# Optimization experiments

Measured on AMD Instinct MI355X. Metric: run time of the kernel, lower is better.

Reference implementation:

```python
import jax, jax.numpy as jnp
import numpy as np

B_COMMITMENT = 1.0


def setup_inputs() -> dict:
    key = jax.random.key(0)
    k1, k2 = jax.random.split(key)
    inpt = jax.random.normal(k1, (16, 1024, 256), dtype=jnp.float32)
    emb_mtrx = jax.random.normal(k2, (256, 8192), dtype=jnp.float32) * 0.05
    return {"inpt": inpt, "emb_mtrx": emb_mtrx}


def reference(inpt, emb_mtrx):
    D = inpt.shape[-1]
    x = inpt.reshape(-1, D)  # [N, D]
    # squared L2 distance to every code: [N, K]
    dist = (
        jnp.sum(x * x, axis=1, keepdims=True)
        - 2.0 * (x @ emb_mtrx)
        + jnp.sum(emb_mtrx * emb_mtrx, axis=0, keepdims=True)
    )
    idx = jnp.argmin(dist, axis=1).reshape(inpt.shape[:-1])  # [B, T]
    q = jnp.take(emb_mtrx.T, idx, axis=0)  # [B, T, D] gather of nearest codes
    l_commitment = jnp.mean((jax.lax.stop_gradient(q) - inpt) ** 2)
    l_codebook = jnp.mean((q - jax.lax.stop_gradient(inpt)) ** 2)
    loss = B_COMMITMENT * l_commitment + l_codebook
    q_st = inpt + jax.lax.stop_gradient(q - inpt)  # straight-through
    return q_st, loss
```

## Files before the change

kernel.cpp:

```cpp
#include <hip/hip_runtime.h>
#include <hip/hip_bf16.h>
#include <cstdint>


typedef __bf16 bf16x8 __attribute__((ext_vector_type(8)));
typedef __bf16 bf16x4 __attribute__((ext_vector_type(4)));
typedef float  f32x16 __attribute__((ext_vector_type(16)));

#define N_ROWS  16384
#define N_CODES 8192
#define DDIM    256
#define NT      16
#define BUFB3   32768
#define NMAX    8192
#define THETA   0.020f

#define P1_LDS   163840
#define P1_EOFF  131072
#define P1_NOFF  155648

#define STAGE16(gptr, lptr) __builtin_amdgcn_global_load_lds( \
    (const __attribute__((address_space(1))) void*)(gptr),    \
    (__attribute__((address_space(3))) void*)(lptr), 16, 0, 0)

#define SBAR() do { asm volatile("" ::: "memory"); \
                    __builtin_amdgcn_s_barrier();  \
                    asm volatile("" ::: "memory"); } while (0)
#define WAITVM(N) asm volatile("s_waitcnt vmcnt(" #N ")" ::: "memory")
#define LGKM0() do { asm volatile("s_waitcnt lgkmcnt(0)" ::: "memory"); \
                     __builtin_amdgcn_sched_barrier(0); } while (0)

__device__ __forceinline__ unsigned mapf(float f) {
  unsigned u = __float_as_uint(f);
  return (u & 0x80000000u) ? ~u : (u | 0x80000000u);
}
__device__ __forceinline__ float unmapf(unsigned u) {
  u = (u & 0x80000000u) ? (u & 0x7fffffffu) : ~u;
  return __uint_as_float(u);
}

__global__ void prep_all_k(const float* __restrict__ x, const float* __restrict__ emb,
                           __bf16* __restrict__ xhi, __bf16* __restrict__ xlo,
                           __bf16* __restrict__ ehi, __bf16* __restrict__ elo,
                           float* __restrict__ enorm) {
  __shared__ float tile[64][65];
  const int b = blockIdx.x;
  const int t = threadIdx.x;
  if (b < 4096) {
    int i = b * 256 + t;
    float4 v = reinterpret_cast<const float4*>(x)[i];
    float a[4] = {v.x, v.y, v.z, v.w};
    bf16x4 h, l;
#pragma unroll
    for (int j = 0; j < 4; ++j) {
      __bf16 hh = (__bf16)a[j];
      h[j] = hh;
      l[j] = (__bf16)(a[j] - (float)hh);
    }
    reinterpret_cast<bf16x4*>(xhi)[i] = h;
    reinterpret_cast<bf16x4*>(xlo)[i] = l;
  } else if (b < 4608) {
    const int pb = b - 4096;
    const int kb = (pb & 127) * 64, db = (pb >> 7) * 64;
    const int tk = t & 63, td = t >> 6;
#pragma unroll
    for (int c = 0; c < 16; ++c) {
      int d = c * 4 + td;
      tile[d][tk] = emb[(size_t)(db + d) * N_CODES + kb + tk];
    }
    __syncthreads();
#pragma unroll
    for (int c = 0; c < 16; ++c) {
      int k = c * 4 + td;
      int d = tk;
      float v = tile[d][k];
      size_t o = (size_t)(kb + k) * DDIM + db + d;
      __bf16 h = (__bf16)v;
      ehi[o] = h;
      elo[o] = (__bf16)(v - (float)h);
    }
  } else {
    int k = (b - 4608) * 256 + t;
    float s = 0.f;
    for (int d = 0; d < DDIM; ++d) {
      float v = emb[(size_t)d * N_CODES + k];
      s += v * v;
    }
    enorm[k] = s;
  }
}

__global__ __launch_bounds__(512, 2) void pass1_k(
    const __bf16* __restrict__ xhi, const __bf16* __restrict__ ehi,
    const float* __restrict__ enorm,
    unsigned long long* __restrict__ k2k, float* __restrict__ k2v) {
  extern __shared__ __align__(16) unsigned char smem[];

  const int tid = threadIdx.x;
  const int wid = tid >> 6, lane = tid & 63;
  const int cg = wid >> 2, rg = wid & 3;
  const int l31 = lane & 31, lh = lane >> 5;

  const int bm = blockIdx.x >> 2;
  const int bnq = blockIdx.x & 3;

  unsigned char* xr = smem;
  unsigned char* eb = smem + P1_EOFF;
  float* enf = (float*)(smem + P1_NOFF);

  const size_t xsrc = (size_t)(bm * 256 + wid * 32 + l31) * 512 + (size_t)lh * 16;
#pragma unroll
  for (int kc = 0; kc < 16; ++kc)
    STAGE16((const char*)xhi + xsrc + kc * 32, xr + (kc * 8 + wid) * 1024);
  STAGE16((const char*)enorm + bnq * 8192 + wid * 1024 + lane * 16,
          smem + P1_NOFF + wid * 1024);
  const size_t esrc0 = (size_t)(bnq * 8 * 256 + wid * 32 + l31) * 512 + (size_t)lh * 16;
  STAGE16((const char*)ehi + esrc0, eb + wid * 1024);
  STAGE16((const char*)ehi + esrc0 + 32, eb + 8192 + wid * 1024);
  WAITVM(1);
  SBAR();

  const int erd = cg * 4096 + lane * 16;

  f32x16 acc[4][2];
#define INIT_ACC(BI) do {                                                      \
  _Pragma("unroll")                                                            \
  for (int c_ = 0; c_ < 4; ++c_) {                                             \
    f32x16 ci_;                                                                \
    _Pragma("unroll")                                                          \
    for (int q_ = 0; q_ < 4; ++q_) {                                           \
      float4 v4_ = *(const float4*)(enf + (BI) * 256 + cg * 128 + c_ * 32 +    \
                                    q_ * 8 + lh * 4);                          \
      ci_[q_ * 4 + 0] = -0.5f * v4_.x; ci_[q_ * 4 + 1] = -0.5f * v4_.y;        \
      ci_[q_ * 4 + 2] = -0.5f * v4_.z; ci_[q_ * 4 + 3] = -0.5f * v4_.w;        \
    }                                                                          \
    acc[c_][0] = ci_; acc[c_][1] = ci_;                                        \
  } } while (0)
  INIT_ACC(0);

  const int rowl = rg * 64 + l31;

#pragma unroll 1
  for (int g = 0; g < 128; ++g) {
    const int s = (g + 2) & 127;
    const size_t esrc = (size_t)((bnq * 8 + (s >> 4)) * 256 + wid * 32 + l31) * 512 +
                        (size_t)(s & 15) * 32 + (size_t)lh * 16;
    STAGE16((const char*)ehi + esrc, eb + ((g + 2) % 3) * 8192 + wid * 1024);

    const unsigned char* rbuf = eb + (g % 3) * 8192;
    const unsigned char* xk = xr + (g & 15) * 8192;
    bf16x8 ef[4], xf[2];
#pragma unroll
    for (int c = 0; c < 4; ++c) ef[c] = *(const bf16x8*)(rbuf + erd + c * 1024);
#pragma unroll
    for (int r = 0; r < 2; ++r)
      xf[r] = *(const bf16x8*)(xk + (rg * 2 + r) * 1024 + lane * 16);

    __builtin_amdgcn_s_setprio(1);
#pragma unroll
    for (int c = 0; c < 4; ++c)
#pragma unroll
      for (int r = 0; r < 2; ++r)
        acc[c][r] = __builtin_amdgcn_mfma_f32_32x32x16_bf16(ef[c], xf[r], acc[c][r], 0, 0, 0);
    __builtin_amdgcn_s_setprio(0);

    WAITVM(1);
    SBAR();

    if ((g & 15) == 15) {
      const int bi = g >> 4;
      const int bn = bnq * 8 + bi;
      const int cbase = bn * 256 + cg * 128 + lh * 4;
      unsigned long long* ek = (unsigned long long*)(eb + (g % 3) * 8192);
      float* ev = (float*)(eb + (g % 3) * 8192 + 2048);
#pragma unroll
      for (int r = 0; r < 2; ++r) {
        float v1 = -3.4e38f, v2 = -3.4e38f;
        unsigned c1 = 0;
#pragma unroll
        for (int c = 0; c < 4; ++c)
#pragma unroll
          for (int q = 0; q < 4; ++q)
#pragma unroll
            for (int rr = 0; rr < 4; ++rr) {
              float v = acc[c][r][q * 4 + rr];
              unsigned cd = (unsigned)(cbase + c * 32 + q * 8 + rr);
              if (v > v1) { v2 = v1; v1 = v; c1 = cd; }
              else if (v > v2) v2 = v;
            }
        unsigned long long key =
            ((unsigned long long)mapf(v1) << 32) | (0xFFFFFFFFu ^ c1);
        unsigned klo = (unsigned)key, khi = (unsigned)(key >> 32);
        unsigned plo = __shfl_xor(klo, 32, 64), phi = __shfl_xor(khi, 32, 64);
        float pv1 = __shfl_xor(v1, 32, 64), pv2 = __shfl_xor(v2, 32, 64);
        unsigned long long pkey = ((unsigned long long)phi << 32) | plo;
        if (pkey > key) { v2 = fmaxf(v1, pv2); v1 = pv1; key = pkey; }
        else { v2 = fmaxf(pv1, v2); }
        SBAR();
        if (cg == 1 && lh == 0) { ek[rowl + r * 32] = key; ev[rowl + r * 32] = v2; }
        SBAR();
        if (cg == 0 && lh == 0) {
          unsigned long long pk = ek[rowl + r * 32];
          float ps2 = ev[rowl + r * 32];
          float nv2;
          if (pk > key) { nv2 = fmaxf(v1, ps2); key = pk; }
          else nv2 = fmaxf(unmapf((unsigned)(pk >> 32)), v2);
          const int grow = bm * 256 + rowl + r * 32;
          k2k[(size_t)bn * N_ROWS + grow] = key;
          k2v[(size_t)bn * N_ROWS + grow] = nv2;
        }
      }
      if (bi < 7) INIT_ACC(bi + 1);
      SBAR();
    }
  }
  WAITVM(0);
}

__global__ void reduce_k(const unsigned long long* __restrict__ k2k,
                         const float* __restrict__ k2v,
                         unsigned long long* __restrict__ keys,
                         unsigned* __restrict__ counter,
                         int* __restrict__ idxlist) {
  const int row = blockIdx.x * 256 + threadIdx.x;
  unsigned long long k = k2k[row];
  float s2 = k2v[row];
#pragma unroll 1
  for (int p = 1; p < 32; ++p) {
    unsigned long long kk = k2k[(size_t)p * N_ROWS + row];
    float ss2 = k2v[(size_t)p * N_ROWS + row];
    if (kk > k) { s2 = fmaxf(unmapf((unsigned)(k >> 32)), ss2); k = kk; }
    else        { s2 = fmaxf(unmapf((unsigned)(kk >> 32)), s2); }
  }
  float v1 = unmapf((unsigned)(k >> 32));
  if (v1 - s2 >= THETA) {
    keys[row] = k;
  } else {
    keys[row] = 0;
    unsigned pos = atomicAdd(counter, 1u);
    if (pos < NMAX) idxlist[pos] = row;
    else keys[row] = k;
  }
}

__global__ void compact_k(const __bf16* __restrict__ xhi, const __bf16* __restrict__ xlo,
                          const int* __restrict__ idxlist, const unsigned* __restrict__ counter,
                          __bf16* __restrict__ xch, __bf16* __restrict__ xcl) {
  const unsigned b = blockIdx.x;
  if (b >= *counter) return;
  const int row = idxlist[b];
  const int lane = threadIdx.x;
  reinterpret_cast<uint2*>(xch)[(size_t)b * 64 + lane] =
      reinterpret_cast<const uint2*>(xhi)[(size_t)row * 64 + lane];
  reinterpret_cast<uint2*>(xcl)[(size_t)b * 64 + lane] =
      reinterpret_cast<const uint2*>(xlo)[(size_t)row * 64 + lane];
}

__global__ __launch_bounds__(512, 2) void rescue_k(
    const __bf16* __restrict__ xch, const __bf16* __restrict__ xcl,
    const __bf16* __restrict__ ehi, const __bf16* __restrict__ elo,
    const float* __restrict__ enorm, unsigned long long* __restrict__ keys,
    const int* __restrict__ idxlist, const unsigned* __restrict__ counter) {
  extern __shared__ __align__(16) unsigned char smem[];

  const int bm = blockIdx.x >> 5;
  const int bn = blockIdx.x & 31;
  const unsigned nf = *counter;
  const int tiles = (int)((nf + 255u) >> 8);
  if (bm >= tiles) return;

  const int tid = threadIdx.x;
  const int wid = tid >> 6, lane = tid & 63;
  const int cg = wid >> 2, rg = wid & 3;
  const int l31 = lane & 31, lh = lane >> 5;

  const int cbase = bn * 256 + cg * 128 + lh * 4;
  f32x16 acc[4][2];
#pragma unroll
  for (int c = 0; c < 4; ++c) {
    f32x16 ci;
#pragma unroll
    for (int q = 0; q < 4; ++q)
#pragma unroll
      for (int r = 0; r < 4; ++r)
        ci[q * 4 + r] = -0.5f * enorm[cbase + c * 32 + q * 8 + r];
    acc[c][0] = ci; acc[c][1] = ci;
  }
  __builtin_amdgcn_sched_barrier(0);

  const size_t aoff = (size_t)(bm * 256 + wid * 32 + l31) * 512 + (size_t)lh * 16;
  const size_t boff = (size_t)(bn * 256 + wid * 32 + l31) * 512 + (size_t)lh * 16;
  const char* pxh = (const char*)xch + aoff;
  const char* pxl = (const char*)xcl + aoff;
  const char* peh = (const char*)ehi + boff;
  const char* pel = (const char*)elo + boff;
  const int dxh = wid * 1024, dxl = 8192 + wid * 1024;
  const int deh = 16384 + wid * 1024, del = 24576 + wid * 1024;

  const int xrd = rg * 2048 + lane * 16;
  const int erd = 16384 + cg * 4096 + lane * 16;

  unsigned char* b0 = smem;
  unsigned char* b1 = smem + BUFB3;
  unsigned char* b2 = smem + 2 * BUFB3;

  STAGE16(pxh, b0 + dxh); STAGE16(peh, b0 + deh);
  STAGE16(pxl, b0 + dxl); STAGE16(pel, b0 + del);
  STAGE16(pxh + 32, b1 + dxh); STAGE16(peh + 32, b1 + deh);
  STAGE16(pxl + 32, b1 + dxl); STAGE16(pel + 32, b1 + del);
  WAITVM(4);
  SBAR();

#pragma unroll 1
  for (int t = 0; t < NT; ++t) {
    int s = t + 2; if (s >= NT) s -= NT;
    const size_t kb = (size_t)s * 32;

    bf16x8 ehf[4], xhf[2];
#pragma unroll
    for (int c = 0; c < 4; ++c) ehf[c] = *(const bf16x8*)(b0 + erd + c * 1024);
#pragma unroll
    for (int r = 0; r < 2; ++r) xhf[r] = *(const bf16x8*)(b0 + xrd + r * 1024);
    STAGE16(pxh + kb, b2 + dxh);
    STAGE16(peh + kb, b2 + deh);
    SBAR();
    LGKM0();
    __builtin_amdgcn_s_setprio(1);
#pragma unroll
    for (int c = 0; c < 4; ++c)
#pragma unroll
      for (int r = 0; r < 2; ++r)
        acc[c][r] = __builtin_amdgcn_mfma_f32_32x32x16_bf16(ehf[c], xhf[r], acc[c][r], 0, 0, 0);
    __builtin_amdgcn_s_setprio(0);
    SBAR();

    bf16x8 xlf[2];
#pragma unroll
    for (int r = 0; r < 2; ++r) xlf[r] = *(const bf16x8*)(b0 + 8192 + xrd + r * 1024);
    STAGE16(pxl + kb, b2 + dxl);
    SBAR();
    LGKM0();
    __builtin_amdgcn_s_setprio(1);
#pragma unroll
    for (int c = 0; c < 4; ++c)
#pragma unroll
      for (int r = 0; r < 2; ++r)
        acc[c][r] = __builtin_amdgcn_mfma_f32_32x32x16_bf16(ehf[c], xlf[r], acc[c][r], 0, 0, 0);
    __builtin_amdgcn_s_setprio(0);
    SBAR();

    bf16x8 elf[4];
#pragma unroll
    for (int c = 0; c < 4; ++c) elf[c] = *(const bf16x8*)(b0 + 8192 + erd + c * 1024);
    STAGE16(pel + kb, b2 + del);
    SBAR();
    LGKM0();
    __builtin_amdgcn_s_setprio(1);
#pragma unroll
    for (int c = 0; c < 4; ++c)
#pragma unroll
      for (int r = 0; r < 2; ++r)
        acc[c][r] = __builtin_amdgcn_mfma_f32_32x32x16_bf16(elf[c], xhf[r], acc[c][r], 0, 0, 0);
    __builtin_amdgcn_s_setprio(0);
    WAITVM(4);
    SBAR();

    unsigned char* bt = b0; b0 = b1; b1 = b2; b2 = bt;
  }
  WAITVM(0);

#pragma unroll
  for (int r = 0; r < 2; ++r) {
    float bv = -3.4e38f;
    unsigned bcode = 0;
#pragma unroll
    for (int c = 0; c < 4; ++c)
#pragma unroll
      for (int q = 0; q < 4; ++q)
#pragma unroll
        for (int rr = 0; rr < 4; ++rr) {
          float v = acc[c][r][q * 4 + rr];
          unsigned cd = (unsigned)(cbase + c * 32 + q * 8 + rr);
          if (v > bv) { bv = v; bcode = cd; }
        }
    unsigned long long key =
        ((unsigned long long)mapf(bv) << 32) | (0xFFFFFFFFu ^ bcode);
    unsigned olo = __shfl_xor((unsigned)key, 32, 64);
    unsigned ohi = __shfl_xor((unsigned)(key >> 32), 32, 64);
    unsigned long long okey = ((unsigned long long)ohi << 32) | olo;
    if (okey > key) key = okey;
    const int crow = bm * 256 + rg * 64 + r * 32 + l31;
    if (lane < 32 && crow < (int)nf)
      atomicMax(&keys[idxlist[crow]], key);
  }
}

__global__ void gather_k(const float* __restrict__ x,
                         const __bf16* __restrict__ ehi, const __bf16* __restrict__ elo,
                         const unsigned long long* __restrict__ keys,
                         float* __restrict__ qout, float* __restrict__ rowsum) {
  const int row = blockIdx.x * 4 + (threadIdx.x >> 6);
  const int lane = threadIdx.x & 63;
  const unsigned low = (unsigned)(keys[row] & 0xffffffffull);
  const int idx = (int)(~low);
  ushort4 h4 = reinterpret_cast<const ushort4*>(ehi + (size_t)idx * DDIM)[lane];
  ushort4 l4 = reinterpret_cast<const ushort4*>(elo + (size_t)idx * DDIM)[lane];
  float4 xv = reinterpret_cast<const float4*>(x + (size_t)row * DDIM)[lane];
  float4 q;
  q.x = __uint_as_float((unsigned)h4.x << 16) + __uint_as_float((unsigned)l4.x << 16);
  q.y = __uint_as_float((unsigned)h4.y << 16) + __uint_as_float((unsigned)l4.y << 16);
  q.z = __uint_as_float((unsigned)h4.z << 16) + __uint_as_float((unsigned)l4.z << 16);
  q.w = __uint_as_float((unsigned)h4.w << 16) + __uint_as_float((unsigned)l4.w << 16);
  reinterpret_cast<float4*>(qout + (size_t)row * DDIM)[lane] = q;
  float dx = q.x - xv.x, dy = q.y - xv.y, dz = q.z - xv.z, dw = q.w - xv.w;
  float s = dx * dx + dy * dy + dz * dz + dw * dw;
#pragma unroll
  for (int mk = 32; mk; mk >>= 1) s += __shfl_xor(s, mk, 64);
  if (lane == 0) rowsum[row] = s;
}

__global__ void loss_k(const float* __restrict__ rowsum, float* __restrict__ out) {
  __shared__ float sm[4];
  const int t = threadIdx.x;
  float s = 0.f;
  for (int j = t; j < N_ROWS; j += 256) s += rowsum[j];
#pragma unroll
  for (int mk = 32; mk; mk >>= 1) s += __shfl_xor(s, mk, 64);
  if ((t & 63) == 0) sm[t >> 6] = s;
  __syncthreads();
  if (t == 0) out[0] = 2.0f * (sm[0] + sm[1] + sm[2] + sm[3]) / (float)(N_ROWS * DDIM);
}

extern "C" void kernel_launch(void* const* d_in, const int* in_sizes, int n_in,
                              void* d_out, int out_size, void* d_ws, size_t ws_size,
                              hipStream_t stream) {
  const float* x   = (const float*)d_in[0];
  const float* emb = (const float*)d_in[1];
  float* qout = (float*)d_out;

  char* w = (char*)d_ws;
  unsigned long long* keys = (unsigned long long*)w;
  float* rowsum   = (float*)(w + 131072);
  unsigned* counter = (unsigned*)(w + 196608);
  int* idxlist    = (int*)(w + 197632);
  __bf16* xhi     = (__bf16*)(w + 262144);
  __bf16* xlo     = xhi + (size_t)N_ROWS * DDIM;
  __bf16* ehi     = xlo + (size_t)N_ROWS * DDIM;
  __bf16* elo     = ehi + (size_t)N_CODES * DDIM;
  float*  enorm   = (float*)(elo + (size_t)N_CODES * DDIM);
  char*   k2base  = (char*)(enorm + N_CODES);
  unsigned long long* k2k = (unsigned long long*)k2base;
  float*  k2v     = (float*)(k2base + 4194304);
  __bf16* xch     = (__bf16*)k2base;
  __bf16* xcl     = (__bf16*)(k2base + 4194304);

  hipFuncSetAttribute((const void*)pass1_k,
                      hipFuncAttributeMaxDynamicSharedMemorySize, P1_LDS);
  hipFuncSetAttribute((const void*)rescue_k,
                      hipFuncAttributeMaxDynamicSharedMemorySize, 3 * BUFB3);

  hipMemsetAsync(counter, 0, sizeof(unsigned), stream);
  prep_all_k<<<4640, 256, 0, stream>>>(x, emb, xhi, xlo, ehi, elo, enorm);
  pass1_k<<<256, 512, P1_LDS, stream>>>(xhi, ehi, enorm, k2k, k2v);
  reduce_k<<<N_ROWS / 256, 256, 0, stream>>>(k2k, k2v, keys, counter, idxlist);
  compact_k<<<NMAX, 64, 0, stream>>>(xhi, xlo, idxlist, counter, xch, xcl);
  rescue_k<<<(NMAX / 256) * 32, 512, 3 * BUFB3, stream>>>(
      xch, xcl, ehi, elo, enorm, keys, idxlist, counter);
  gather_k<<<N_ROWS / 4, 256, 0, stream>>>(x, ehi, elo, keys, qout, rowsum);
  loss_k<<<1, 256, 0, stream>>>(rowsum, qout + (size_t)N_ROWS * DDIM);
}
```

Measured before the change: 203.9 us.

## Shrink pass1 tiles to 128 rows with 4 waves and double-buffered code staging

Pass1 now launches 512 blocks of 256 threads, each handling 128 input rows instead of 256, which halves the LDS footprint. Code-chunk staging drops from a triple buffer to a double buffer and waits for all loads before each barrier. The enorm values are read straight from global memory instead of being staged in LDS, and block indices are swizzled so neighbouring blocks share input rows. The aim is more resident blocks and better cache locality, at the cost of less reuse of each code tile per block and less prefetch slack.

```diff
diff --git a/kernel.cpp b/kernel.cpp
--- a/kernel.cpp
+++ b/kernel.cpp
@@ -15,9 +15,8 @@
 #define NMAX    8192
 #define THETA   0.020f
 
-#define P1_LDS   163840
-#define P1_EOFF  131072
-#define P1_NOFF  155648
+#define P1_LDS   81920
+#define P1_EOFF  65536
 
 #define STAGE16(gptr, lptr) __builtin_amdgcn_global_load_lds( \
     (const __attribute__((address_space(1))) void*)(gptr),    \
@@ -90,7 +89,7 @@
   }
 }
 
-__global__ __launch_bounds__(512, 2) void pass1_k(
+__global__ __launch_bounds__(256, 2) void pass1_k(
     const __bf16* __restrict__ xhi, const __bf16* __restrict__ ehi,
     const float* __restrict__ enorm,
     unsigned long long* __restrict__ k2k, float* __restrict__ k2v) {
@@ -98,39 +97,39 @@
 
   const int tid = threadIdx.x;
   const int wid = tid >> 6, lane = tid & 63;
-  const int cg = wid >> 2, rg = wid & 3;
+  const int rg = wid & 1, cg = wid >> 1;
   const int l31 = lane & 31, lh = lane >> 5;
 
-  const int bm = blockIdx.x >> 2;
-  const int bnq = blockIdx.x & 3;
+  const int orig = blockIdx.x;
+  const int j = orig >> 3;
+  const int bm = (orig & 7) * 16 + (j & 15);
+  const int bnq = j >> 4;
 
   unsigned char* xr = smem;
   unsigned char* eb = smem + P1_EOFF;
-  float* enf = (float*)(smem + P1_NOFF);
-
-  const size_t xsrc = (size_t)(bm * 256 + wid * 32 + l31) * 512 + (size_t)lh * 16;
+
+  const size_t xsrc = (size_t)(bm * 128 + wid * 32 + l31) * 512 + (size_t)lh * 16;
 #pragma unroll
   for (int kc = 0; kc < 16; ++kc)
-    STAGE16((const char*)xhi + xsrc + kc * 32, xr + (kc * 8 + wid) * 1024);
-  STAGE16((const char*)enorm + bnq * 8192 + wid * 1024 + lane * 16,
-          smem + P1_NOFF + wid * 1024);
-  const size_t esrc0 = (size_t)(bnq * 8 * 256 + wid * 32 + l31) * 512 + (size_t)lh * 16;
-  STAGE16((const char*)ehi + esrc0, eb + wid * 1024);
-  STAGE16((const char*)ehi + esrc0 + 32, eb + 8192 + wid * 1024);
-  WAITVM(1);
+    STAGE16((const char*)xhi + xsrc + kc * 32, xr + (kc * 4 + wid) * 1024);
+#pragma unroll
+  for (int u = 0; u < 2; ++u) {
+    const int eu = wid * 2 + u;
+    const size_t es = (size_t)(bnq * 2048 + eu * 32 + l31) * 512 + (size_t)lh * 16;
+    STAGE16((const char*)ehi + es, eb + eu * 1024);
+  }
+  WAITVM(0);
   SBAR();
 
-  const int erd = cg * 4096 + lane * 16;
-
   f32x16 acc[4][2];
-#define INIT_ACC(BI) do {                                                      \
+#define INIT_ACC(P) do {                                                       \
   _Pragma("unroll")                                                            \
   for (int c_ = 0; c_ < 4; ++c_) {                                             \
     f32x16 ci_;                                                                \
     _Pragma("unroll")                                                          \
     for (int q_ = 0; q_ < 4; ++q_) {                                           \
-      float4 v4_ = *(const float4*)(enf + (BI) * 256 + cg * 128 + c_ * 32 +    \
-                                    q_ * 8 + lh * 4);                          \
+      float4 v4_ = *(const float4*)(enorm + bnq * 2048 + (P) * 256 +           \
+                                    cg * 128 + c_ * 32 + q_ * 8 + lh * 4);     \
       ci_[q_ * 4 + 0] = -0.5f * v4_.x; ci_[q_ * 4 + 1] = -0.5f * v4_.y;        \
       ci_[q_ * 4 + 2] = -0.5f * v4_.z; ci_[q_ * 4 + 3] = -0.5f * v4_.w;        \
     }                                                                          \
@@ -138,20 +137,24 @@
   } } while (0)
   INIT_ACC(0);
 
-  const int rowl = rg * 64 + l31;
-
 #pragma unroll 1
   for (int g = 0; g < 128; ++g) {
-    const int s = (g + 2) & 127;
-    const size_t esrc = (size_t)((bnq * 8 + (s >> 4)) * 256 + wid * 32 + l31) * 512 +
+    const int s = (g + 1) & 127;
+    unsigned char* wb = eb + ((g + 1) & 1) * 8192;
+#pragma unroll
+    for (int u = 0; u < 2; ++u) {
+      const int eu = wid * 2 + u;
+      const size_t es = (size_t)(bnq * 2048 + (s >> 4) * 256 + eu * 32 + l31) * 512 +
                         (size_t)(s & 15) * 32 + (size_t)lh * 16;
-    STAGE16((const char*)ehi + esrc, eb + ((g + 2) % 3) * 8192 + wid * 1024);
-
-    const unsigned char* rbuf = eb + (g % 3) * 8192;
-    const unsigned char* xk = xr + (g & 15) * 8192;
+      STAGE16((const char*)ehi + es, wb + eu * 1024);
+    }
+
+    const unsigned char* rbuf = eb + (g & 1) * 8192;
+    const unsigned char* xk = xr + (g & 15) * 4096;
     bf16x8 ef[4], xf[2];
 #pragma unroll
-    for (int c = 0; c < 4; ++c) ef[c] = *(const bf16x8*)(rbuf + erd + c * 1024);
+    for (int c = 0; c < 4; ++c)
+      ef[c] = *(const bf16x8*)(rbuf + (cg * 4 + c) * 1024 + lane * 16);
 #pragma unroll
     for (int r = 0; r < 2; ++r)
       xf[r] = *(const bf16x8*)(xk + (rg * 2 + r) * 1024 + lane * 16);
@@ -164,15 +167,15 @@
         acc[c][r] = __builtin_amdgcn_mfma_f32_32x32x16_bf16(ef[c], xf[r], acc[c][r], 0, 0, 0);
     __builtin_amdgcn_s_setprio(0);
 
-    WAITVM(1);
+    WAITVM(0);
     SBAR();
 
     if ((g & 15) == 15) {
       const int bi = g >> 4;
       const int bn = bnq * 8 + bi;
       const int cbase = bn * 256 + cg * 128 + lh * 4;
-      unsigned long long* ek = (unsigned long long*)(eb + (g % 3) * 8192);
-      float* ev = (float*)(eb + (g % 3) * 8192 + 2048);
+      unsigned long long* ek = (unsigned long long*)(eb + (g & 1) * 8192);
+      float* ev = (float*)(eb + (g & 1) * 8192 + 2048);
 #pragma unroll
       for (int r = 0; r < 2; ++r) {
         float v1 = -3.4e38f, v2 = -3.4e38f;
@@ -196,16 +199,17 @@
         unsigned long long pkey = ((unsigned long long)phi << 32) | plo;
         if (pkey > key) { v2 = fmaxf(v1, pv2); v1 = pv1; key = pkey; }
         else { v2 = fmaxf(pv1, v2); }
+        const int rowl = rg * 64 + r * 32 + l31;
         SBAR();
-        if (cg == 1 && lh == 0) { ek[rowl + r * 32] = key; ev[rowl + r * 32] = v2; }
+        if (cg == 1 && lh == 0) { ek[rowl] = key; ev[rowl] = v2; }
         SBAR();
         if (cg == 0 && lh == 0) {
-          unsigned long long pk = ek[rowl + r * 32];
-          float ps2 = ev[rowl + r * 32];
+          unsigned long long pk = ek[rowl];
+          float ps2 = ev[rowl];
           float nv2;
           if (pk > key) { nv2 = fmaxf(v1, ps2); key = pk; }
           else nv2 = fmaxf(unmapf((unsigned)(pk >> 32)), v2);
-          const int grow = bm * 256 + rowl + r * 32;
+          const int grow = bm * 128 + rowl;
           k2k[(size_t)bn * N_ROWS + grow] = key;
           k2v[(size_t)bn * N_ROWS + grow] = nv2;
         }
@@ -461,7 +465,7 @@
 
   hipMemsetAsync(counter, 0, sizeof(unsigned), stream);
   prep_all_k<<<4640, 256, 0, stream>>>(x, emb, xhi, xlo, ehi, elo, enorm);
-  pass1_k<<<256, 512, P1_LDS, stream>>>(xhi, ehi, enorm, k2k, k2v);
+  pass1_k<<<512, 256, P1_LDS, stream>>>(xhi, ehi, enorm, k2k, k2v);
   reduce_k<<<N_ROWS / 256, 256, 0, stream>>>(k2k, k2v, keys, counter, idxlist);
   compact_k<<<NMAX, 64, 0, stream>>>(xhi, xlo, idxlist, counter, xch, xcl);
   rescue_k<<<(NMAX / 256) * 32, 512, 3 * BUFB3, stream>>>(
```

Result: slower. 216.4 us (+6.1%).
